# Optimization experiments

Hardware: AMD Instinct MI355X
Metric: run time of the kernel (lower is better)

Reference implementation:

```python
import jax, jax.numpy as jnp
import numpy as np

N_NODES = 100000
N_EDGES = 1600000
D_IN = 64
D_OUT = 64


def setup_inputs() -> dict:
    key = jax.random.key(0)
    k1, k2, k3, k4 = jax.random.split(key, 4)
    x = jax.random.normal(k1, (N_NODES, D_IN), dtype=jnp.float32)
    src = jax.random.randint(k2, (N_EDGES,), 0, N_NODES, dtype=jnp.int32)
    dst = jax.random.randint(k3, (N_EDGES,), 0, N_NODES, dtype=jnp.int32)
    W = jax.random.normal(k4, (D_OUT, D_IN), dtype=jnp.float32) / np.sqrt(D_IN)
    b = jnp.zeros((D_OUT,), dtype=jnp.float32)
    return {"x": x, "src": src, "dst": dst, "W": W, "b": b}


def reference(x, src, dst, W, b):
    # DGL SAGEConv with 'gcn' aggregator:
    #   h_neigh = (sum_{j in N_in(i)} x_j + x_i) / (in_degree(i) + 1)
    #   out     = h_neigh @ W^T + b
    N = x.shape[0]
    # gather source features and scatter-add into destination nodes  [N, D_IN]
    neigh_sum = jax.ops.segment_sum(x[src], dst, num_segments=N)
    deg = jax.ops.segment_sum(jnp.ones_like(dst, dtype=x.dtype), dst, num_segments=N)
    h_neigh = (neigh_sum + x) / (deg + 1.0)[:, None]
    return h_neigh @ W.T + b
```

## Files before the change

### kernel.cpp

```cpp
#include <hip/hip_runtime.h>

#define D 64
#define BSH 7
#define BSZ 128
#define NBMAX 1024
#define TILE 8192
#define CAP  3072
#define SRTC (CAP + 1024 + 8)

typedef unsigned int   uint;
typedef unsigned short ushort_t;
typedef __attribute__((ext_vector_type(8))) short bf16x8;
typedef __attribute__((ext_vector_type(4))) float f32x4;

__device__ __forceinline__ ushort_t f2bf(float f) {
    uint u = __float_as_uint(f);
    u += 0x7FFFu + ((u >> 16) & 1u);
    return (ushort_t)(u >> 16);
}

__global__ __launch_bounds__(256) void k_bhist(
    const int* __restrict__ dst, int* __restrict__ bucketCount,
    int* __restrict__ blockBase, const float4* __restrict__ x4,
    uint4* __restrict__ xb4, int n8, int nb, int n_edges)
{
    __shared__ int hist[NBMAX];
    const int tid = threadIdx.x;
    for (int i = tid; i < nb; i += 256) hist[i] = 0;
    __syncthreads();

    if (blockIdx.x == 0 && tid < 8) {
        uint4 z; z.x = z.y = z.z = z.w = 0u;
        xb4[n8 + tid] = z;
    }

    {
        const int chunk = (n8 + gridDim.x - 1) / gridDim.x;
        const int lo = blockIdx.x * chunk;
        const int hi = min(n8, lo + chunk);
        for (int t = lo + tid; t < hi; t += 256) {
            float4 a = x4[t * 2];
            float4 c = x4[t * 2 + 1];
            uint4 o;
            o.x = (uint)f2bf(a.x) | ((uint)f2bf(a.y) << 16);
            o.y = (uint)f2bf(a.z) | ((uint)f2bf(a.w) << 16);
            o.z = (uint)f2bf(c.x) | ((uint)f2bf(c.y) << 16);
            o.w = (uint)f2bf(c.z) | ((uint)f2bf(c.w) << 16);
            xb4[t] = o;
        }
    }

    const int e0 = blockIdx.x * TILE;
    const int n4 = n_edges >> 2;
    const int4* dst4 = (const int4*)dst;
#pragma unroll
    for (int k = 0; k < TILE / 1024; ++k) {
        int i4 = (e0 >> 2) + k * 256 + tid;
        if (i4 < n4) {
            int4 d = dst4[i4];
            atomicAdd(&hist[d.x >> BSH], 1);
            atomicAdd(&hist[d.y >> BSH], 1);
            atomicAdd(&hist[d.z >> BSH], 1);
            atomicAdd(&hist[d.w >> BSH], 1);
        }
    }
    if (blockIdx.x == gridDim.x - 1) {
        for (int e = (n4 << 2) + tid; e < n_edges; e += 256)
            atomicAdd(&hist[dst[e] >> BSH], 1);
    }
    __syncthreads();
    for (int i = tid; i < nb; i += 256)
        blockBase[(size_t)blockIdx.x * nb + i] = atomicAdd(&bucketCount[i], hist[i]);
}

__global__ __launch_bounds__(1024) void k_bscan(
    const int* __restrict__ bucketCount, int* __restrict__ bucketBase, int nb)
{
    __shared__ int s[1024];
    const int tid = threadIdx.x;
    int v = (tid < nb) ? bucketCount[tid] : 0;
    s[tid] = v;
    __syncthreads();
    for (int off = 1; off < 1024; off <<= 1) {
        int t = (tid >= off) ? s[tid - off] : 0;
        __syncthreads();
        s[tid] += t;
        __syncthreads();
    }
    if (tid <= nb) bucketBase[tid] = s[tid] - v;
}

__global__ __launch_bounds__(256) void k_bscatter(
    const int* __restrict__ src, const int* __restrict__ dst,
    const int* __restrict__ bucketBase, const int* __restrict__ blockBase,
    int* __restrict__ packed, int nb, int n_edges)
{
    __shared__ int cur[NBMAX];
    const int tid = threadIdx.x;
    const int blk = blockIdx.x;
    for (int i = tid; i < nb; i += 256)
        cur[i] = bucketBase[i] + blockBase[(size_t)blk * nb + i];
    __syncthreads();

    const int e0 = blk * TILE;
    const int n4 = n_edges >> 2;
    const int4* src4 = (const int4*)src;
    const int4* dst4 = (const int4*)dst;
#pragma unroll
    for (int k = 0; k < TILE / 1024; ++k) {
        int i4 = (e0 >> 2) + k * 256 + tid;
        if (i4 < n4) {
            int4 sv = src4[i4];
            int4 dv = dst4[i4];
            int p;
            p = atomicAdd(&cur[dv.x >> BSH], 1); packed[p] = sv.x | ((dv.x & (BSZ-1)) << 24);
            p = atomicAdd(&cur[dv.y >> BSH], 1); packed[p] = sv.y | ((dv.y & (BSZ-1)) << 24);
            p = atomicAdd(&cur[dv.z >> BSH], 1); packed[p] = sv.z | ((dv.z & (BSZ-1)) << 24);
            p = atomicAdd(&cur[dv.w >> BSH], 1); packed[p] = sv.w | ((dv.w & (BSZ-1)) << 24);
        }
    }
    if (blk == gridDim.x - 1) {
        for (int e = (n4 << 2) + tid; e < n_edges; e += 256) {
            int p = atomicAdd(&cur[dst[e] >> BSH], 1);
            packed[p] = src[e] | ((dst[e] & (BSZ-1)) << 24);
        }
    }
}

__global__ __launch_bounds__(512, 8) void k_aggcsr(
    const int* __restrict__ packed, const int* __restrict__ bucketBase,
    const uint2* __restrict__ xb2, const float* __restrict__ W,
    const float* __restrict__ bvec, float* __restrict__ out, int n_nodes)
{
    __shared__ int raw[CAP];
    __shared__ int srt[SRTC];
    __shared__ ushort_t Wl[64 * 64];
    __shared__ int ldeg[BSZ];
    __shared__ int lofs[BSZ];
    __shared__ int cur[BSZ];

    const int tid = threadIdx.x;
    const int bucket = blockIdx.x;
    const int ebase = bucketBase[bucket];
    const int ecnt  = bucketBase[bucket + 1] - ebase;
    const bool fits = (ecnt <= CAP);
    const uint nmax = (uint)(n_nodes - 1);
    const int zrow = n_nodes;

    {
        const int o = tid >> 3;
        const int j = (tid & 7) * 8;
        const float* wp = W + o * 64 + j;
        float4 wa = *(const float4*)wp;
        float4 wb = *(const float4*)(wp + 4);
        uint4 w4;
        w4.x = (uint)f2bf(wa.x) | ((uint)f2bf(wa.y) << 16);
        w4.y = (uint)f2bf(wa.z) | ((uint)f2bf(wa.w) << 16);
        w4.z = (uint)f2bf(wb.x) | ((uint)f2bf(wb.y) << 16);
        w4.w = (uint)f2bf(wb.z) | ((uint)f2bf(wb.w) << 16);
        *(uint4*)((char*)Wl + o * 128 + ((j * 2) ^ ((o & 7) << 4))) = w4;
    }
    if (tid < BSZ) ldeg[tid] = 0;
    __syncthreads();

    if (fits) {
        for (int i = tid; i < ecnt; i += 512) {
            int pk = packed[ebase + i];
            raw[i] = pk;
            atomicAdd(&ldeg[((uint)pk) >> 24], 1);
        }
    } else {
        for (int i = tid; i < ecnt; i += 512)
            atomicAdd(&ldeg[((uint)packed[ebase + i]) >> 24], 1);
    }
    __syncthreads();

    {
        int v = 0;
        if (tid < BSZ) { v = (ldeg[tid] + 7) & ~7; lofs[tid] = v; }
        __syncthreads();
        for (int off = 1; off < BSZ; off <<= 1) {
            int t = (tid < BSZ && tid >= off) ? lofs[tid - off] : 0;
            __syncthreads();
            if (tid < BSZ) lofs[tid] += t;
            __syncthreads();
        }
        if (tid < BSZ) { int e = lofs[tid] - v; lofs[tid] = e; cur[tid] = e; }
    }
    __syncthreads();

    if (fits) {
        for (int i = tid; i < ecnt; i += 512) {
            int pk = raw[i];
            int pos = atomicAdd(&cur[((uint)pk) >> 24], 1);
            srt[pos] = pk & 0x00FFFFFF;
        }
        if (tid < BSZ) {
            int base = lofs[tid] + ldeg[tid];
            int end  = lofs[tid] + ((ldeg[tid] + 7) & ~7);
            for (int i = base; i < end; ++i) srt[i] = zrow;
        }
    }
    __syncthreads();

    const int wave = tid >> 6;
    const int lane = tid & 63;
    const int g    = lane >> 4;
    const int fq   = lane & 15;

#define CVLO(u) __uint_as_float((u) << 16)
#define CVHI(u) __uint_as_float((u) & 0xFFFF0000u)

    const uint2* __restrict__ xbf = xb2 + fq;

    uint2 hreg[4];
#pragma unroll
    for (int p = 0; p < 4; ++p) { hreg[p].x = 0u; hreg[p].y = 0u; }

#pragma unroll
    for (int p = 0; p < 4; ++p) {
        const int nl = wave * 16 + p * 4 + g;
        const int node = (bucket << BSH) + nl;
        const bool valid = (node < n_nodes);
        const int cnt = valid ? ldeg[nl] : 0;
        const int eb  = valid ? lofs[nl] : 0;
        const int pc  = (cnt + 7) & ~7;

        float s0 = 0.f, s1 = 0.f, s2 = 0.f, s3 = 0.f;

        if (fits) {
            for (int i = 0; i < pc; i += 8) {
                uint vv[8];
#pragma unroll
                for (int k = 0; k < 8; ++k) vv[k] = (uint)srt[eb + i + k];
                uint2 A[8];
#pragma unroll
                for (int k = 0; k < 8; ++k)
                    A[k] = xbf[(size_t)vv[k] * 16];
#pragma unroll
                for (int k = 0; k < 8; ++k) {
                    s0 += CVLO(A[k].x);
                    s1 += CVHI(A[k].x);
                    s2 += CVLO(A[k].y);
                    s3 += CVHI(A[k].y);
                }
            }
        } else {
            const int nlm = valid ? nl : -1;
            for (int i = 0; i < ecnt; ++i) {
                int pk = packed[ebase + i];
                float m0 = ((int)(((uint)pk) >> 24) == nlm) ? 1.0f : 0.0f;
                uint2 A0 = xbf[(size_t)min((uint)(pk & 0x00FFFFFF), nmax) * 16];
                s0 = fmaf(m0, CVLO(A0.x), s0);
                s1 = fmaf(m0, CVHI(A0.x), s1);
                s2 = fmaf(m0, CVLO(A0.y), s2);
                s3 = fmaf(m0, CVHI(A0.y), s3);
            }
        }

        if (valid) {
            uint2 xv = xbf[(size_t)node * 16];
            float rinv = 1.0f / (float)(cnt + 1);
            float h0 = (s0 + CVLO(xv.x)) * rinv;
            float h1 = (s1 + CVHI(xv.x)) * rinv;
            float h2 = (s2 + CVLO(xv.y)) * rinv;
            float h3 = (s3 + CVHI(xv.y)) * rinv;
            hreg[p].x = (uint)f2bf(h0) | ((uint)f2bf(h1) << 16);
            hreg[p].y = (uint)f2bf(h2) | ((uint)f2bf(h3) << 16);
        }
    }
#undef CVLO
#undef CVHI

    __syncthreads();

    char* hwb = (char*)srt + wave * 2048;
#pragma unroll
    for (int p = 0; p < 4; ++p) {
        int nl = p * 4 + g;
        *(uint2*)(hwb + nl * 128 + ((fq * 8) ^ ((nl & 7) << 4))) = hreg[p];
    }

    const int m  = lane & 15;
    const int kg = lane >> 4;
    bf16x8 a0 = *(const bf16x8*)(hwb + m * 128 + (((kg * 16)     ) ^ ((m & 7) << 4)));
    bf16x8 a1 = *(const bf16x8*)(hwb + m * 128 + (((64 + kg * 16)) ^ ((m & 7) << 4)));

    const int node0 = (bucket << BSH) + wave * 16;
#pragma unroll
    for (int c = 0; c < 4; ++c) {
        const int o = c * 16 + m;
        bf16x8 b0 = *(const bf16x8*)((char*)Wl + o * 128 + (((kg * 16)     ) ^ ((o & 7) << 4)));
        bf16x8 b1 = *(const bf16x8*)((char*)Wl + o * 128 + (((64 + kg * 16)) ^ ((o & 7) << 4)));
        f32x4 acc = {0.f, 0.f, 0.f, 0.f};
        acc = __builtin_amdgcn_mfma_f32_16x16x32_bf16(a0, b0, acc, 0, 0, 0);
        acc = __builtin_amdgcn_mfma_f32_16x16x32_bf16(a1, b1, acc, 0, 0, 0);
        const float bias = bvec[o];
#pragma unroll
        for (int r = 0; r < 4; ++r) {
            int row = node0 + kg * 4 + r;
            if (row < n_nodes)
                out[(size_t)row * 64 + o] = acc[r] + bias;
        }
    }
}

extern "C" void kernel_launch(void* const* d_in, const int* in_sizes, int n_in,
                              void* d_out, int out_size, void* d_ws, size_t ws_size,
                              hipStream_t stream)
{
    const float* x   = (const float*)d_in[0];
    const int*   src = (const int*)d_in[1];
    const int*   dst = (const int*)d_in[2];
    const float* W   = (const float*)d_in[3];
    const float* b   = (const float*)d_in[4];
    float* out = (float*)d_out;

    const int n_nodes = in_sizes[0] / D;
    const int n_edges = in_sizes[1];
    const int nb  = (n_nodes + BSZ - 1) >> BSH;
    const int nbA = (n_edges + TILE - 1) / TILE;

    ushort_t* xb = (ushort_t*)d_ws;
    int* bucketCount = (int*)(xb + (size_t)(n_nodes + 1) * D);
    int* bucketBase  = bucketCount + NBMAX;
    int* blockBase   = bucketBase + NBMAX + 1;
    int* packed      = blockBase + (size_t)nbA * nb;

    hipMemsetAsync(bucketCount, 0, NBMAX * sizeof(int), stream);

    const int n8 = n_nodes * D / 8;
    k_bhist   <<<nbA, 256, 0, stream>>>(dst, bucketCount, blockBase,
                                        (const float4*)x, (uint4*)xb, n8, nb, n_edges);
    k_bscan   <<<1,  1024, 0, stream>>>(bucketCount, bucketBase, nb);
    k_bscatter<<<nbA, 256, 0, stream>>>(src, dst, bucketBase, blockBase, packed, nb, n_edges);
    k_aggcsr  <<<nb,  512, 0, stream>>>(packed, bucketBase, (const uint2*)xb,
                                        W, b, out, n_nodes);
}
```

Before: 78.41 us.

## Halve bucket size and fold bucket scan into scatter kernel

Shrinks destination buckets from 128 to 64 nodes, doubling the number of aggregation blocks. Each wave now aggregates 8 nodes, and the MFMA projection runs on 4 of the 8 waves after a shared staging step. The separate single-block scan kernel is removed: every scatter block computes the bucket prefix sum redundantly, and block 0 writes bucketBase. This removes one launch and improves load balance, but adds redundant scan work per block, one extra barrier, and idle waves during the matmul.

```diff
diff --git a/kernel.cpp b/kernel.cpp
--- a/kernel.cpp
+++ b/kernel.cpp
@@ -1,12 +1,12 @@
 #include <hip/hip_runtime.h>
 
 #define D 64
-#define BSH 7
-#define BSZ 128
-#define NBMAX 1024
+#define BSH 6
+#define BSZ 64
+#define NBMAX 2048
 #define TILE 8192
-#define CAP  3072
-#define SRTC (CAP + 1024 + 8)
+#define CAP  1536
+#define SRTC (CAP + BSZ * 8 + 8)
 
 typedef unsigned int   uint;
 typedef unsigned short ushort_t;
@@ -73,33 +73,51 @@
         blockBase[(size_t)blockIdx.x * nb + i] = atomicAdd(&bucketCount[i], hist[i]);
 }
 
-__global__ __launch_bounds__(1024) void k_bscan(
-    const int* __restrict__ bucketCount, int* __restrict__ bucketBase, int nb)
-{
-    __shared__ int s[1024];
-    const int tid = threadIdx.x;
-    int v = (tid < nb) ? bucketCount[tid] : 0;
-    s[tid] = v;
-    __syncthreads();
-    for (int off = 1; off < 1024; off <<= 1) {
-        int t = (tid >= off) ? s[tid - off] : 0;
-        __syncthreads();
-        s[tid] += t;
-        __syncthreads();
-    }
-    if (tid <= nb) bucketBase[tid] = s[tid] - v;
-}
-
 __global__ __launch_bounds__(256) void k_bscatter(
     const int* __restrict__ src, const int* __restrict__ dst,
-    const int* __restrict__ bucketBase, const int* __restrict__ blockBase,
-    int* __restrict__ packed, int nb, int n_edges)
+    const int* __restrict__ bucketCount, const int* __restrict__ blockBase,
+    int* __restrict__ bucketBase, int* __restrict__ packed,
+    int nb, int n_edges)
 {
+    __shared__ int sc[NBMAX];
     __shared__ int cur[NBMAX];
+    __shared__ int ts[256];
     const int tid = threadIdx.x;
     const int blk = blockIdx.x;
+
+    {
+        const int base = tid * 8;
+        int v[8];
+#pragma unroll
+        for (int k = 0; k < 8; ++k)
+            v[k] = (base + k < nb) ? bucketCount[base + k] : 0;
+        int tsum = 0;
+#pragma unroll
+        for (int k = 0; k < 8; ++k) tsum += v[k];
+        ts[tid] = tsum;
+        __syncthreads();
+        for (int off = 1; off < 256; off <<= 1) {
+            int t = (tid >= off) ? ts[tid - off] : 0;
+            __syncthreads();
+            ts[tid] += t;
+            __syncthreads();
+        }
+        int run = ts[tid] - tsum;
+#pragma unroll
+        for (int k = 0; k < 8; ++k) {
+            if (base + k < nb) sc[base + k] = run;
+            run += v[k];
+        }
+    }
+    __syncthreads();
+
+    if (blk == 0) {
+        for (int i = tid; i <= nb; i += 256)
+            bucketBase[i] = (i < nb) ? sc[i] : n_edges;
+    }
+
     for (int i = tid; i < nb; i += 256)
-        cur[i] = bucketBase[i] + blockBase[(size_t)blk * nb + i];
+        cur[i] = sc[i] + blockBase[(size_t)blk * nb + i];
     __syncthreads();
 
     const int e0 = blk * TILE;
@@ -213,13 +231,13 @@
 
     const uint2* __restrict__ xbf = xb2 + fq;
 
-    uint2 hreg[4];
-#pragma unroll
-    for (int p = 0; p < 4; ++p) { hreg[p].x = 0u; hreg[p].y = 0u; }
-
-#pragma unroll
-    for (int p = 0; p < 4; ++p) {
-        const int nl = wave * 16 + p * 4 + g;
+    uint2 hreg[2];
+#pragma unroll
+    for (int p = 0; p < 2; ++p) { hreg[p].x = 0u; hreg[p].y = 0u; }
+
+#pragma unroll
+    for (int p = 0; p < 2; ++p) {
+        const int nl = wave * 8 + p * 4 + g;
         const int node = (bucket << BSH) + nl;
         const bool valid = (node < n_nodes);
         const int cnt = valid ? ldeg[nl] : 0;
@@ -274,33 +292,37 @@
 
     __syncthreads();
 
-    char* hwb = (char*)srt + wave * 2048;
-#pragma unroll
-    for (int p = 0; p < 4; ++p) {
-        int nl = p * 4 + g;
-        *(uint2*)(hwb + nl * 128 + ((fq * 8) ^ ((nl & 7) << 4))) = hreg[p];
-    }
-
-    const int m  = lane & 15;
-    const int kg = lane >> 4;
-    bf16x8 a0 = *(const bf16x8*)(hwb + m * 128 + (((kg * 16)     ) ^ ((m & 7) << 4)));
-    bf16x8 a1 = *(const bf16x8*)(hwb + m * 128 + (((64 + kg * 16)) ^ ((m & 7) << 4)));
-
-    const int node0 = (bucket << BSH) + wave * 16;
-#pragma unroll
-    for (int c = 0; c < 4; ++c) {
-        const int o = c * 16 + m;
-        bf16x8 b0 = *(const bf16x8*)((char*)Wl + o * 128 + (((kg * 16)     ) ^ ((o & 7) << 4)));
-        bf16x8 b1 = *(const bf16x8*)((char*)Wl + o * 128 + (((64 + kg * 16)) ^ ((o & 7) << 4)));
-        f32x4 acc = {0.f, 0.f, 0.f, 0.f};
-        acc = __builtin_amdgcn_mfma_f32_16x16x32_bf16(a0, b0, acc, 0, 0, 0);
-        acc = __builtin_amdgcn_mfma_f32_16x16x32_bf16(a1, b1, acc, 0, 0, 0);
-        const float bias = bvec[o];
-#pragma unroll
-        for (int r = 0; r < 4; ++r) {
-            int row = node0 + kg * 4 + r;
-            if (row < n_nodes)
-                out[(size_t)row * 64 + o] = acc[r] + bias;
+    char* hstage = (char*)srt;
+#pragma unroll
+    for (int p = 0; p < 2; ++p) {
+        int nl = wave * 8 + p * 4 + g;
+        *(uint2*)(hstage + nl * 128 + ((fq * 8) ^ ((nl & 7) << 4))) = hreg[p];
+    }
+    __syncthreads();
+
+    if (wave < 4) {
+        char* hwb = hstage + wave * 2048;
+        const int m  = lane & 15;
+        const int kg = lane >> 4;
+        bf16x8 a0 = *(const bf16x8*)(hwb + m * 128 + (((kg * 16)     ) ^ ((m & 7) << 4)));
+        bf16x8 a1 = *(const bf16x8*)(hwb + m * 128 + (((64 + kg * 16)) ^ ((m & 7) << 4)));
+
+        const int node0 = (bucket << BSH) + wave * 16;
+#pragma unroll
+        for (int c = 0; c < 4; ++c) {
+            const int o = c * 16 + m;
+            bf16x8 b0 = *(const bf16x8*)((char*)Wl + o * 128 + (((kg * 16)     ) ^ ((o & 7) << 4)));
+            bf16x8 b1 = *(const bf16x8*)((char*)Wl + o * 128 + (((64 + kg * 16)) ^ ((o & 7) << 4)));
+            f32x4 acc = {0.f, 0.f, 0.f, 0.f};
+            acc = __builtin_amdgcn_mfma_f32_16x16x32_bf16(a0, b0, acc, 0, 0, 0);
+            acc = __builtin_amdgcn_mfma_f32_16x16x32_bf16(a1, b1, acc, 0, 0, 0);
+            const float bias = bvec[o];
+#pragma unroll
+            for (int r = 0; r < 4; ++r) {
+                int row = node0 + kg * 4 + r;
+                if (row < n_nodes)
+                    out[(size_t)row * 64 + o] = acc[r] + bias;
+            }
         }
     }
 }
@@ -332,8 +354,8 @@
     const int n8 = n_nodes * D / 8;
     k_bhist   <<<nbA, 256, 0, stream>>>(dst, bucketCount, blockBase,
                                         (const float4*)x, (uint4*)xb, n8, nb, n_edges);
-    k_bscan   <<<1,  1024, 0, stream>>>(bucketCount, bucketBase, nb);
-    k_bscatter<<<nbA, 256, 0, stream>>>(src, dst, bucketBase, blockBase, packed, nb, n_edges);
+    k_bscatter<<<nbA, 256, 0, stream>>>(src, dst, bucketCount, blockBase,
+                                        bucketBase, packed, nb, n_edges);
     k_aggcsr  <<<nb,  512, 0, stream>>>(packed, bucketBase, (const uint2*)xb,
                                         W, b, out, n_nodes);
 }
```

Result: no change. 79.66 us (+1.6%).
